# Kernel optimization log

Measured on AMD Instinct MI355X. Metric: run time of the kernel, lower is better.

## Reference

```python
import jax, jax.numpy as jnp
import numpy as np

D_MODEL, D_KEY, D_VALUE, H = 1024, 64, 64, 16
B, S = 4, 2048

def setup_inputs() -> dict:
    key = jax.random.key(0)
    ks = jax.random.split(key, 11)
    sd = 1.0 / np.sqrt(D_MODEL)
    return {
        "queries": jax.random.normal(ks[0], (B, S, D_MODEL), jnp.float32),
        "keys": jax.random.normal(ks[1], (B, S, D_MODEL), jnp.float32),
        "values": jax.random.normal(ks[2], (B, S, D_MODEL), jnp.float32),
        "Wq": jax.random.normal(ks[3], (D_MODEL, H * D_KEY), jnp.float32) * sd,
        "bq": jax.random.normal(ks[4], (H * D_KEY,), jnp.float32) * 0.01,
        "Wk": jax.random.normal(ks[5], (D_MODEL, H * D_KEY), jnp.float32) * sd,
        "bk": jax.random.normal(ks[6], (H * D_KEY,), jnp.float32) * 0.01,
        "Wv": jax.random.normal(ks[7], (D_MODEL, H * D_VALUE), jnp.float32) * sd,
        "bv": jax.random.normal(ks[8], (H * D_VALUE,), jnp.float32) * 0.01,
        "Wo": jax.random.normal(ks[9], (H * D_VALUE, D_MODEL), jnp.float32) * sd,
        "bo": jax.random.normal(ks[10], (D_MODEL,), jnp.float32) * 0.01,
    }

def reference(queries, keys, values, Wq, bq, Wk, bk, Wv, bv, Wo, bo):
    bs, nq, _ = queries.shape
    nk = keys.shape[1]
    # projections -> [b, h, s, d]
    q = (queries @ Wq + bq).reshape(bs, nq, H, D_KEY).transpose(0, 2, 1, 3)
    k = (keys @ Wk + bk).reshape(bs, nk, H, D_KEY).transpose(0, 2, 1, 3)
    v = (values @ Wv + bv).reshape(bs, nk, H, D_VALUE).transpose(0, 2, 1, 3)
    att = jnp.einsum('bhqd,bhkd->bhqk', q, k) / np.sqrt(D_KEY).astype(np.float32)
    att = jax.nn.softmax(att, axis=-1)  # dropout is identity in eval mode
    out = jnp.einsum('bhqk,bhkd->bhqd', att, v)
    out = out.transpose(0, 2, 1, 3).reshape(bs, nq, H * D_VALUE)
    return out @ Wo + bo
```

## Files before the change

kernel.cpp:

```cpp
#include <hip/hip_runtime.h>
#include <hip/hip_bf16.h>
#include <stdint.h>

#define DM 1024
#define DKH 64
#define NH 16
#define NB 4
#define SEQ 2048

typedef __attribute__((ext_vector_type(8))) short bf16x8;
typedef __attribute__((ext_vector_type(4))) short bf16x4;
typedef __attribute__((ext_vector_type(8))) unsigned short ushort8;
typedef __attribute__((ext_vector_type(4))) float f32x4;

__device__ inline unsigned short f2bf(float f) {
  union { float f; unsigned u; } c; c.f = f;
  unsigned u = c.u;
  u += 0x7fff + ((u >> 16) & 1);
  return (unsigned short)(u >> 16);
}

#define GLOAD16(dst, ptr, OFF)                                              \
  asm volatile("global_load_dwordx4 %0, %1, off offset:" #OFF               \
               : "=v"(dst) : "v"(ptr))
#define GLOAD8(dst, ptr, OFF)                                               \
  asm volatile("global_load_dwordx2 %0, %1, off offset:" #OFF               \
               : "=v"(dst) : "v"(ptr))

#define WAITV(N)                                            \
  do {                                                      \
    asm volatile("s_waitcnt vmcnt(" #N ")" ::: "memory");   \
    __builtin_amdgcn_sched_barrier(0);                      \
  } while (0)

__device__ inline void glds16(const unsigned short* g, unsigned short* l) {
  __builtin_amdgcn_global_load_lds(
      (const __attribute__((address_space(1))) unsigned int*)g,
      (__attribute__((address_space(3))) unsigned int*)l, 16, 0, 0);
}

__device__ inline void mfma16x16x16(f32x4& acc, bf16x4 a, bf16x4 b) {
  asm("v_mfma_f32_16x16x16_bf16 %0, %1, %2, %0" : "+v"(acc) : "v"(a), "v"(b));
}

__global__ __launch_bounds__(256) void acast(const float* __restrict__ A,
                                             unsigned short* __restrict__ O) {
  size_t i = ((size_t)blockIdx.x * 256 + threadIdx.x) * 8;
  const float* p = A + i;
  float4 x = *reinterpret_cast<const float4*>(p);
  float4 y = *reinterpret_cast<const float4*>(p + 4);
  ushort8 v;
  v[0] = f2bf(x.x); v[1] = f2bf(x.y); v[2] = f2bf(x.z); v[3] = f2bf(x.w);
  v[4] = f2bf(y.x); v[5] = f2bf(y.y); v[6] = f2bf(y.z); v[7] = f2bf(y.w);
  *reinterpret_cast<ushort8*>(O + i) = v;
}

__global__ __launch_bounds__(256) void wcast_all(const float* __restrict__ W0,
                                                 const float* __restrict__ W1,
                                                 const float* __restrict__ W2,
                                                 const float* __restrict__ W3,
                                                 unsigned short* __restrict__ Wt0,
                                                 unsigned short* __restrict__ Wt1,
                                                 unsigned short* __restrict__ Wt2,
                                                 unsigned short* __restrict__ Wt3) {
  __shared__ float tile[32][33];
  int z = blockIdx.z;
  const float* W = z == 0 ? W0 : z == 1 ? W1 : z == 2 ? W2 : W3;
  unsigned short* Wt = z == 0 ? Wt0 : z == 1 ? Wt1 : z == 2 ? Wt2 : Wt3;
  int bk = blockIdx.x * 32, bn = blockIdx.y * 32;
  int tx = threadIdx.x & 31, ty = threadIdx.x >> 5;
#pragma unroll
  for (int i = 0; i < 4; ++i)
    tile[ty + 8 * i][tx] = W[(size_t)(bk + ty + 8 * i) * DM + bn + tx];
  __syncthreads();
#pragma unroll
  for (int i = 0; i < 4; ++i)
    Wt[(size_t)(bn + ty + 8 * i) * DM + bk + tx] = f2bf(tile[tx][ty + 8 * i]);
}

template <int EPI>
__global__ __launch_bounds__(256) void gemm_bf16(const unsigned short* __restrict__ A,
                                                 const unsigned short* __restrict__ Bt,
                                                 const float* __restrict__ bias,
                                                 void* __restrict__ Cv, float scale) {
  __shared__ __align__(16) unsigned short As[128][32];
  __shared__ __align__(16) unsigned short Bs[128][32];
  const int K = DM;
  int t = threadIdx.x;
  int wave = t >> 6, lane = t & 63;
  int wr = wave >> 1, wc = wave & 1;
  int l15 = lane & 15, g = lane >> 4;
  int bid = blockIdx.x;
  int xcd = bid & 7, ii = bid >> 3;
  int tn = ii >> 3;
  int tm = ((ii & 7) << 3) | xcd;
  int rowBase = tm * 128, colBase = tn * 128;

  f32x4 acc[4][4];
#pragma unroll
  for (int mi = 0; mi < 4; ++mi)
#pragma unroll
    for (int ni = 0; ni < 4; ++ni) acc[mi][ni] = (f32x4){0.f, 0.f, 0.f, 0.f};

  const unsigned short* sa0 =
      A + (size_t)(rowBase + wave * 16 + (lane >> 2)) * K + (lane & 3) * 8;
  const unsigned short* sa1 = sa0 + (size_t)64 * K;
  const unsigned short* sb0 =
      Bt + (size_t)(colBase + wave * 16 + (lane >> 2)) * K + (lane & 3) * 8;
  const unsigned short* sb1 = sb0 + (size_t)64 * K;
  unsigned short* la0 = &As[wave * 16][0];
  unsigned short* la1 = &As[64 + wave * 16][0];
  unsigned short* lb0 = &Bs[wave * 16][0];
  unsigned short* lb1 = &Bs[64 + wave * 16][0];

  for (int kt = 0; kt < K; kt += 32) {
    __syncthreads();
    glds16(sa0, la0);
    glds16(sa1, la1);
    glds16(sb0, lb0);
    glds16(sb1, lb1);
    sa0 += 32; sa1 += 32; sb0 += 32; sb1 += 32;
    WAITV(0);
    __syncthreads();

    bf16x8 af[4], bfr[4];
#pragma unroll
    for (int mi = 0; mi < 4; ++mi)
      af[mi] = *reinterpret_cast<const bf16x8*>(&As[wr * 64 + mi * 16 + l15][g * 8]);
#pragma unroll
    for (int ni = 0; ni < 4; ++ni)
      bfr[ni] = *reinterpret_cast<const bf16x8*>(&Bs[wc * 64 + ni * 16 + l15][g * 8]);
#pragma unroll
    for (int mi = 0; mi < 4; ++mi)
#pragma unroll
      for (int ni = 0; ni < 4; ++ni)
        acc[mi][ni] = __builtin_amdgcn_mfma_f32_16x16x32_bf16(af[mi], bfr[ni],
                                                              acc[mi][ni], 0, 0, 0);
  }

#pragma unroll
  for (int ni = 0; ni < 4; ++ni) {
    int col = colBase + wc * 64 + ni * 16 + l15;
    float bvv = bias[col];
#pragma unroll
    for (int mi = 0; mi < 4; ++mi) {
#pragma unroll
      for (int r = 0; r < 4; ++r) {
        int row = rowBase + wr * 64 + mi * 16 + g * 4 + r;
        float val = (acc[mi][ni][r] + bvv) * scale;
        if (EPI == 3) {
          ((float*)Cv)[(size_t)row * DM + col] = val;
        } else {
          int b_ = row >> 11, s_ = row & 2047;
          int h_ = col >> 6, d_ = col & 63;
          size_t hb = (size_t)(b_ * NH + h_) * (SEQ * DKH);
          size_t idx;
          if (EPI == 0) {
            idx = hb + (size_t)s_ * DKH + d_;
          } else if (EPI == 1) {
            idx = hb + (size_t)(s_ >> 4) * 1024 + (d_ >> 5) * 512 +
                  ((d_ >> 3) & 3) * 128 + (s_ & 15) * 8 + (d_ & 7);
          } else {
            idx = hb + (size_t)(s_ >> 5) * 2048 + ((s_ >> 4) & 1) * 1024 +
                  (d_ >> 4) * 256 + ((s_ >> 2) & 3) * 64 + (d_ & 15) * 4 + (s_ & 3);
          }
          ((unsigned short*)Cv)[idx] = f2bf(val);
        }
      }
    }
  }
}

__global__ __launch_bounds__(256) void attn_fwd(const unsigned short* __restrict__ Qb,
                                                const unsigned short* __restrict__ Kp_,
                                                const unsigned short* __restrict__ Vp_,
                                                unsigned short* __restrict__ AO) {
  int t = threadIdx.x;
  int wave = t >> 6, lane = t & 63;
  int l15 = lane & 15, g = lane >> 4;
  int bid = blockIdx.x;
  int xcd = bid & 7, j = bid >> 3;
  int bh = (xcd << 3) | (j >> 4);
  int qtile = j & 15;
  const size_t baseH = (size_t)bh * SEQ * DKH;
  int q0 = qtile * 128 + wave * 32;

  bf16x8 aQ[2][2];
#pragma unroll
  for (int qf = 0; qf < 2; ++qf)
#pragma unroll
    for (int dh = 0; dh < 2; ++dh)
      aQ[qf][dh] = *reinterpret_cast<const bf16x8*>(
          Qb + baseH + (size_t)(q0 + qf * 16 + l15) * DKH + dh * 32 + g * 8);

  float lsum[2] = {0.f, 0.f};
  f32x4 accO[2][4];
#pragma unroll
  for (int qf = 0; qf < 2; ++qf)
#pragma unroll
    for (int dt = 0; dt < 4; ++dt) accO[qf][dt] = (f32x4){0.f, 0.f, 0.f, 0.f};

  const unsigned short* kp = Kp_ + baseH + g * 128 + l15 * 8;
  const unsigned short* vp = Vp_ + baseH + g * 64 + l15 * 4;

  bf16x8 k0[2][2], k1[2][2], k2[2][2];
  bf16x4 v0[2][4], v1[2][4], v2[2][4];
  bf16x4 pf[2][2];

#define ISSUE_K(buf)                                  \
  do {                                                \
    GLOAD16(buf[0][0], kp, 0);                        \
    GLOAD16(buf[0][1], kp, 1024);                     \
    GLOAD16(buf[1][0], kp, 2048);                     \
    GLOAD16(buf[1][1], kp, 3072);                     \
    kp += 2048;                                       \
  } while (0)
#define ISSUE_V(buf)                                  \
  do {                                                \
    GLOAD8(buf[0][0], vp, 0);                         \
    GLOAD8(buf[0][1], vp, 512);                       \
    GLOAD8(buf[0][2], vp, 1024);                      \
    GLOAD8(buf[0][3], vp, 1536);                      \
    GLOAD8(buf[1][0], vp, 2048);                      \
    GLOAD8(buf[1][1], vp, 2560);                      \
    GLOAD8(buf[1][2], vp, 3072);                      \
    GLOAD8(buf[1][3], vp, 3584);                      \
    vp += 2048;                                       \
  } while (0)

  const f32x4 ZOFF = (f32x4){-16.f, -16.f, -16.f, -16.f};

  auto qksm = [&](const bf16x8 (&kf)[2][2]) {
    f32x4 sc[2][2];
#pragma unroll
    for (int qf = 0; qf < 2; ++qf)
#pragma unroll
      for (int tt = 0; tt < 2; ++tt) {
        f32x4 z = ZOFF;
#pragma unroll
        for (int dh = 0; dh < 2; ++dh)
          z = __builtin_amdgcn_mfma_f32_16x16x32_bf16(kf[tt][dh], aQ[qf][dh], z, 0, 0, 0);
        sc[qf][tt] = z;
      }
#pragma unroll
    for (int qf = 0; qf < 2; ++qf) {
      float pv[8];
#pragma unroll
      for (int tt = 0; tt < 2; ++tt)
#pragma unroll
        for (int r = 0; r < 4; ++r)
          pv[tt * 4 + r] = __builtin_amdgcn_exp2f(sc[qf][tt][r]);
      lsum[qf] +=
          ((pv[0] + pv[1]) + (pv[2] + pv[3])) + ((pv[4] + pv[5]) + (pv[6] + pv[7]));
#pragma unroll
      for (int tt = 0; tt < 2; ++tt) {
        unsigned w0, w1;
        asm("v_cvt_pk_bf16_f32 %0, %1, %2"
            : "=v"(w0) : "v"(pv[tt * 4 + 0]), "v"(pv[tt * 4 + 1]));
        asm("v_cvt_pk_bf16_f32 %0, %1, %2"
            : "=v"(w1) : "v"(pv[tt * 4 + 2]), "v"(pv[tt * 4 + 3]));
        union { unsigned u[2]; bf16x4 v; } pk;
        pk.u[0] = w0; pk.u[1] = w1;
        pf[qf][tt] = pk.v;
      }
    }
  };

  auto pvstep = [&](const bf16x4 (&vf)[2][4]) {
#pragma unroll
    for (int qf = 0; qf < 2; ++qf)
#pragma unroll
      for (int tt = 0; tt < 2; ++tt)
#pragma unroll
        for (int dt = 0; dt < 4; ++dt)
          mfma16x16x16(accO[qf][dt], vf[tt][dt], pf[qf][tt]);
  };

  ISSUE_K(k0); ISSUE_V(v0);
  ISSUE_K(k1); ISSUE_V(v1);
  ISSUE_K(k2); ISSUE_V(v2);

  for (int it = 0; it < 21; ++it) {
    WAITV(32); qksm(k0); WAITV(24); pvstep(v0); ISSUE_K(k0); ISSUE_V(v0);
    WAITV(32); qksm(k1); WAITV(24); pvstep(v1); ISSUE_K(k1); ISSUE_V(v1);
    WAITV(32); qksm(k2); WAITV(24); pvstep(v2); ISSUE_K(k2); ISSUE_V(v2);
  }
  WAITV(32); qksm(k0); WAITV(24); pvstep(v0);
  WAITV(0);
#undef ISSUE_K
#undef ISSUE_V

  int b_ = bh >> 4, h_ = bh & 15;
#pragma unroll
  for (int qf = 0; qf < 2; ++qf) {
    float ls = lsum[qf];
    ls += __shfl_xor(ls, 16);
    ls += __shfl_xor(ls, 32);
    float inv = 1.f / ls;
    int sq = q0 + qf * 16 + l15;
#pragma unroll
    for (int dt = 0; dt < 4; ++dt)
#pragma unroll
      for (int r = 0; r < 4; ++r) {
        float val = accO[qf][dt][r] * inv;
        AO[(size_t)(b_ * SEQ + sq) * DM + h_ * DKH + dt * 16 + g * 4 + r] = f2bf(val);
      }
  }
}

extern "C" void kernel_launch(void* const* d_in, const int* in_sizes, int n_in,
                              void* d_out, int out_size, void* d_ws, size_t ws_size,
                              hipStream_t stream) {
  (void)in_sizes; (void)n_in; (void)out_size; (void)ws_size;
  const float* queries = (const float*)d_in[0];
  const float* keys = (const float*)d_in[1];
  const float* values = (const float*)d_in[2];
  const float* Wq = (const float*)d_in[3];
  const float* bq = (const float*)d_in[4];
  const float* Wk = (const float*)d_in[5];
  const float* bk = (const float*)d_in[6];
  const float* Wv = (const float*)d_in[7];
  const float* bv = (const float*)d_in[8];
  const float* Wo = (const float*)d_in[9];
  const float* bo = (const float*)d_in[10];
  float* out = (float*)d_out;

  char* ws = (char*)d_ws;
  unsigned short* wt_q = (unsigned short*)(ws + 0 * (1u << 21));
  unsigned short* wt_k = (unsigned short*)(ws + 1 * (1u << 21));
  unsigned short* wt_v = (unsigned short*)(ws + 2 * (1u << 21));
  unsigned short* wt_o = (unsigned short*)(ws + 3 * (1u << 21));
  unsigned short* Qb = (unsigned short*)(ws + (8u << 20));
  unsigned short* Kb = (unsigned short*)(ws + (24u << 20));
  unsigned short* Vt = (unsigned short*)(ws + (40u << 20));
  unsigned short* AO = (unsigned short*)(ws + (56u << 20));

  const float SQ = 0.125f * 1.4426950408889634f;

  wcast_all<<<dim3(32, 32, 4), 256, 0, stream>>>(Wq, Wk, Wv, Wo,
                                                 wt_q, wt_k, wt_v, wt_o);
  acast<<<4096, 256, 0, stream>>>(queries, AO);
  gemm_bf16<0><<<512, 256, 0, stream>>>(AO, wt_q, bq, Qb, SQ);
  acast<<<4096, 256, 0, stream>>>(keys, AO);
  gemm_bf16<1><<<512, 256, 0, stream>>>(AO, wt_k, bk, Kb, 1.0f);
  acast<<<4096, 256, 0, stream>>>(values, AO);
  gemm_bf16<2><<<512, 256, 0, stream>>>(AO, wt_v, bv, Vt, 1.0f);
  attn_fwd<<<1024, 256, 0, stream>>>(Qb, Kb, Vt, AO);
  gemm_bf16<3><<<512, 256, 0, stream>>>(AO, wt_o, bo, out, 1.0f);
}
```

Measured before the change: 249.1 us.

## Repack V layout for 16-byte loads and raise MFMA wave priority

```diff
diff --git a/kernel.cpp b/kernel.cpp
--- a/kernel.cpp
+++ b/kernel.cpp
@@ -13,6 +13,8 @@
 typedef __attribute__((ext_vector_type(8))) unsigned short ushort8;
 typedef __attribute__((ext_vector_type(4))) float f32x4;
 
+union S8 { bf16x8 w; bf16x4 h[2]; };
+
 __device__ inline unsigned short f2bf(float f) {
   union { float f; unsigned u; } c; c.f = f;
   unsigned u = c.u;
@@ -22,9 +24,6 @@
 
 #define GLOAD16(dst, ptr, OFF)                                              \
   asm volatile("global_load_dwordx4 %0, %1, off offset:" #OFF               \
-               : "=v"(dst) : "v"(ptr))
-#define GLOAD8(dst, ptr, OFF)                                               \
-  asm volatile("global_load_dwordx2 %0, %1, off offset:" #OFF               \
                : "=v"(dst) : "v"(ptr))
 
 #define WAITV(N)                                            \
@@ -161,8 +160,9 @@
             idx = hb + (size_t)(s_ >> 4) * 1024 + (d_ >> 5) * 512 +
                   ((d_ >> 3) & 3) * 128 + (s_ & 15) * 8 + (d_ & 7);
           } else {
-            idx = hb + (size_t)(s_ >> 5) * 2048 + ((s_ >> 4) & 1) * 1024 +
-                  (d_ >> 4) * 256 + ((s_ >> 2) & 3) * 64 + (d_ & 15) * 4 + (s_ & 3);
+            idx = hb + (size_t)(s_ >> 5) * 2048 + (d_ >> 4) * 512 +
+                  ((s_ >> 2) & 3) * 128 + (d_ & 15) * 8 + ((s_ >> 4) & 1) * 4 +
+                  (s_ & 3);
           }
           ((unsigned short*)Cv)[idx] = f2bf(val);
         }
@@ -201,10 +201,10 @@
     for (int dt = 0; dt < 4; ++dt) accO[qf][dt] = (f32x4){0.f, 0.f, 0.f, 0.f};
 
   const unsigned short* kp = Kp_ + baseH + g * 128 + l15 * 8;
-  const unsigned short* vp = Vp_ + baseH + g * 64 + l15 * 4;
+  const unsigned short* vp = Vp_ + baseH + (size_t)lane * 8;
 
   bf16x8 k0[2][2], k1[2][2], k2[2][2];
-  bf16x4 v0[2][4], v1[2][4], v2[2][4];
+  S8 v0[4], v1[4], v2[4];
   bf16x4 pf[2][2];
 
 #define ISSUE_K(buf)                                  \
@@ -217,14 +217,10 @@
   } while (0)
 #define ISSUE_V(buf)                                  \
   do {                                                \
-    GLOAD8(buf[0][0], vp, 0);                         \
-    GLOAD8(buf[0][1], vp, 512);                       \
-    GLOAD8(buf[0][2], vp, 1024);                      \
-    GLOAD8(buf[0][3], vp, 1536);                      \
-    GLOAD8(buf[1][0], vp, 2048);                      \
-    GLOAD8(buf[1][1], vp, 2560);                      \
-    GLOAD8(buf[1][2], vp, 3072);                      \
-    GLOAD8(buf[1][3], vp, 3584);                      \
+    GLOAD16(buf[0].w, vp, 0);                         \
+    GLOAD16(buf[1].w, vp, 1024);                      \
+    GLOAD16(buf[2].w, vp, 2048);                      \
+    GLOAD16(buf[3].w, vp, 3072);                      \
     vp += 2048;                                       \
   } while (0)
 
@@ -232,6 +228,7 @@
 
   auto qksm = [&](const bf16x8 (&kf)[2][2]) {
     f32x4 sc[2][2];
+    __builtin_amdgcn_s_setprio(1);
 #pragma unroll
     for (int qf = 0; qf < 2; ++qf)
 #pragma unroll
@@ -242,6 +239,7 @@
           z = __builtin_amdgcn_mfma_f32_16x16x32_bf16(kf[tt][dh], aQ[qf][dh], z, 0, 0, 0);
         sc[qf][tt] = z;
       }
+    __builtin_amdgcn_s_setprio(0);
 #pragma unroll
     for (int qf = 0; qf < 2; ++qf) {
       float pv[8];
@@ -266,14 +264,16 @@
     }
   };
 
-  auto pvstep = [&](const bf16x4 (&vf)[2][4]) {
+  auto pvstep = [&](const S8 (&vf)[4]) {
+    __builtin_amdgcn_s_setprio(1);
 #pragma unroll
     for (int qf = 0; qf < 2; ++qf)
 #pragma unroll
       for (int tt = 0; tt < 2; ++tt)
 #pragma unroll
         for (int dt = 0; dt < 4; ++dt)
-          mfma16x16x16(accO[qf][dt], vf[tt][dt], pf[qf][tt]);
+          mfma16x16x16(accO[qf][dt], vf[dt].h[tt], pf[qf][tt]);
+    __builtin_amdgcn_s_setprio(0);
   };
 
   ISSUE_K(k0); ISSUE_V(v0);
@@ -281,11 +281,11 @@
   ISSUE_K(k2); ISSUE_V(v2);
 
   for (int it = 0; it < 21; ++it) {
-    WAITV(32); qksm(k0); WAITV(24); pvstep(v0); ISSUE_K(k0); ISSUE_V(v0);
-    WAITV(32); qksm(k1); WAITV(24); pvstep(v1); ISSUE_K(k1); ISSUE_V(v1);
-    WAITV(32); qksm(k2); WAITV(24); pvstep(v2); ISSUE_K(k2); ISSUE_V(v2);
+    WAITV(20); qksm(k0); WAITV(16); pvstep(v0); ISSUE_K(k0); ISSUE_V(v0);
+    WAITV(20); qksm(k1); WAITV(16); pvstep(v1); ISSUE_K(k1); ISSUE_V(v1);
+    WAITV(20); qksm(k2); WAITV(16); pvstep(v2); ISSUE_K(k2); ISSUE_V(v2);
   }
-  WAITV(32); qksm(k0); WAITV(24); pvstep(v0);
+  WAITV(20); qksm(k0); WAITV(16); pvstep(v0);
   WAITV(0);
 #undef ISSUE_K
 #undef ISSUE_V
```

Result: faster. 233.7 us (-6.2%).
